# Performance work log

Measured on AMD Instinct MI355X. Metric: run time of the kernel, lower is better.

The kernel has to match this reference:

```python
import jax, jax.numpy as jnp
import numpy as np

USER_NUM = 100000
ITEM_NUM = 100000
N_NODES = USER_NUM + ITEM_NUM
EMB = 64
NNZ = 4000000
N_LAYERS = 3


def setup_inputs() -> dict:
    key = jax.random.key(0)
    k1, k2, k3, k4, k5 = jax.random.split(key, 5)
    # xavier-ish init for embeddings
    scale = np.sqrt(6.0 / (USER_NUM + EMB)).astype(np.float32)
    user_emb = jax.random.uniform(k1, (USER_NUM, EMB), jnp.float32, -scale, scale)
    item_emb = jax.random.uniform(k2, (ITEM_NUM, EMB), jnp.float32, -scale, scale)
    # COO sparse normalized adjacency: values ~ 1/deg scale
    adj_row = jax.random.randint(k3, (NNZ,), 0, N_NODES, dtype=jnp.int64)
    adj_col = jax.random.randint(k4, (NNZ,), 0, N_NODES, dtype=jnp.int64)
    adj_val = jax.random.uniform(k5, (NNZ,), jnp.float32) * (1.0 / 20.0)
    return {"user_emb": user_emb, "item_emb": item_emb,
            "adj_row": adj_row, "adj_col": adj_col, "adj_val": adj_val}


def _spmm(adj_row, adj_col, adj_val, x):
    # y[r] = sum_{e: row[e]==r} val[e] * x[col[e]]   (COO SpMM)
    msg = adj_val[:, None] * x[adj_col]  # [nnz, EMB]
    return jax.ops.segment_sum(msg, adj_row, num_segments=N_NODES)


def reference(user_emb, item_emb, adj_row, adj_col, adj_val):
    ego = jnp.concatenate([user_emb, item_emb], axis=0)  # [N, EMB]
    acc = jnp.zeros_like(ego)
    for _ in range(N_LAYERS):
        ego = _spmm(adj_row, adj_col, adj_val, ego)
        acc = acc + ego
    final = acc / N_LAYERS  # mean over stacked layer outputs
    return final[:USER_NUM], final[USER_NUM:]
```

## Files before the change

kernel.cpp:

```cpp
#include <hip/hip_runtime.h>
#include <hip/hip_fp16.h>

#define EMB 64
#define BROWS 128
#define BSHIFT 7
#define LDSN 2048
#define CHUNK 16384
#define SORT_CAP 5120

typedef int   iv4 __attribute__((ext_vector_type(4)));
typedef float fv4 __attribute__((ext_vector_type(4)));
typedef unsigned uv2 __attribute__((ext_vector_type(2)));

__global__ __launch_bounds__(1024) void bucket_hist(const int* __restrict__ rows,
                                                    int* __restrict__ counts,
                                                    int nnz, int nbuck) {
    __shared__ int lc[LDSN];
    for (int i = threadIdx.x; i < LDSN; i += 1024) lc[i] = 0;
    __syncthreads();
    int stride = gridDim.x * blockDim.x;
    int tid = blockIdx.x * blockDim.x + threadIdx.x;
    int n4 = nnz >> 2;
    for (int q = tid; q < n4; q += stride) {
        iv4 r = __builtin_nontemporal_load((const iv4*)rows + q);
        atomicAdd(&lc[r.x >> BSHIFT], 1);
        atomicAdd(&lc[r.y >> BSHIFT], 1);
        atomicAdd(&lc[r.z >> BSHIFT], 1);
        atomicAdd(&lc[r.w >> BSHIFT], 1);
    }
    int base = n4 << 2;
    if (tid < (nnz - base)) atomicAdd(&lc[rows[base + tid] >> BSHIFT], 1);
    __syncthreads();
    for (int i = threadIdx.x; i < nbuck; i += 1024) {
        int v = lc[i];
        if (v) atomicAdd(&counts[i], v);
    }
}

__global__ void scan_buckets(const int* __restrict__ counts, int* __restrict__ bstart,
                             int* __restrict__ cursor, int nbuck) {
    __shared__ int lds[256];
    int tid = threadIdx.x;
    int run = 0;
    for (int base = 0; base < nbuck; base += 256) {
        int idx = base + tid;
        int v = (idx < nbuck) ? counts[idx] : 0;
        int x = v;
        lds[tid] = x; __syncthreads();
        for (int off = 1; off < 256; off <<= 1) {
            int t = (tid >= off) ? lds[tid - off] : 0;
            __syncthreads();
            x += t; lds[tid] = x; __syncthreads();
        }
        if (idx < nbuck) { int ex = run + x - v; bstart[idx] = ex; cursor[idx] = ex; }
        int tot = lds[255];
        __syncthreads();
        run += tot;
    }
    if (tid == 0) bstart[nbuck] = run;
}

__global__ __launch_bounds__(1024) void bucket_scatter(
        const int* __restrict__ rows, const int* __restrict__ cols,
        const float* __restrict__ vals, int* __restrict__ cursor,
        int2* __restrict__ packed, int nnz) {
    __shared__ int lc[LDSN];
    __shared__ int lbase[LDSN];
    int base = blockIdx.x * CHUNK;
    int end = min(base + CHUNK, nnz);
    for (int i = threadIdx.x; i < LDSN; i += 1024) lc[i] = 0;
    __syncthreads();
    for (int i = base + threadIdx.x; i < end; i += 1024)
        atomicAdd(&lc[rows[i] >> BSHIFT], 1);
    __syncthreads();
    for (int i = threadIdx.x; i < LDSN; i += 1024) {
        int v = lc[i];
        lbase[i] = v ? atomicAdd(&cursor[i], v) : 0;
        lc[i] = 0;
    }
    __syncthreads();
    for (int i = base + threadIdx.x; i < end; i += 1024) {
        int r = rows[i];
        int bk = r >> BSHIFT;
        int slot = lbase[bk] + atomicAdd(&lc[bk], 1);
        packed[slot] = make_int2(cols[i] | ((r & (BROWS - 1)) << 18),
                                 __float_as_int(vals[i]));
    }
}

__global__ __launch_bounds__(512) void sort_bucket(
        int2* __restrict__ packed, const int* __restrict__ bstart,
        int* __restrict__ offs, int n_rows, int nbuck) {
    __shared__ int2 ebuf[SORT_CAP];
    __shared__ int cnt[BROWS];
    __shared__ int coff[BROWS];
    int b = blockIdx.x;
    int s = bstart[b], e = bstart[b + 1];
    int sz = e - s;
    int tid = threadIdx.x;
    if (tid < BROWS) cnt[tid] = 0;
    __syncthreads();
    for (int i = tid; i < sz; i += 512) {
        int2 ed = packed[s + i];
        ebuf[i] = ed;
        atomicAdd(&cnt[(ed.x >> 18) & (BROWS - 1)], 1);
    }
    __syncthreads();
    int v = (tid < BROWS) ? cnt[tid] : 0;
    if (tid < BROWS) coff[tid] = v;
    __syncthreads();
    for (int off = 1; off < BROWS; off <<= 1) {
        int add = (tid < BROWS && tid >= off) ? coff[tid - off] : 0;
        __syncthreads();
        if (tid < BROWS) coff[tid] += add;
        __syncthreads();
    }
    if (tid < BROWS) {
        int ex = coff[tid] - v;
        cnt[tid] = ex;
        int row = (b << BSHIFT) + tid;
        if (row < n_rows) offs[row] = s + ex;
    }
    if (b == nbuck - 1 && tid == 0) offs[n_rows] = e;
    __syncthreads();
    for (int i = tid; i < sz; i += 512) {
        int2 ed = ebuf[i];
        int rl = (ed.x >> 18) & (BROWS - 1);
        int pos = atomicAdd(&cnt[rl], 1);
        packed[s + pos] = make_int2(ed.x & 0x3FFFF, ed.y);
    }
}

__global__ __launch_bounds__(256) void cast_concat_half(
        const float* __restrict__ a, const float* __restrict__ b,
        int na4, int ntot4, __half* __restrict__ o) {
    int stride = gridDim.x * blockDim.x;
    for (int i = blockIdx.x * blockDim.x + threadIdx.x; i < ntot4; i += stride) {
        fv4 v = (i < na4) ? ((const fv4*)a)[i] : ((const fv4*)b)[i - na4];
        __half2 h0 = __floats2half2_rn(v.x, v.y);
        __half2 h1 = __floats2half2_rn(v.z, v.w);
        uv2 w;
        w.x = *(unsigned*)&h0;
        w.y = *(unsigned*)&h1;
        *((uv2*)o + i) = w;
    }
}

__global__ __launch_bounds__(256) void spmm_row_h(
        const int* __restrict__ offs, const int2* __restrict__ packed,
        const __half* __restrict__ xh,
        __half* __restrict__ yh, float* __restrict__ out, int n_rows, int mode) {
    int wid = (blockIdx.x * blockDim.x + threadIdx.x) >> 6;
    if (wid >= n_rows) return;
    int lane = threadIdx.x & 63;
    int r = __builtin_amdgcn_readfirstlane(wid);
    int s = offs[r];
    int e = offs[r + 1];
    const unsigned long long* pk = (const unsigned long long*)packed;
    float a0 = 0.f, a1 = 0.f, a2 = 0.f, a3 = 0.f;
    float a4 = 0.f, a5 = 0.f, a6 = 0.f, a7 = 0.f;
    int k = s;
    for (; k + 7 < e; k += 8) {
        unsigned long long w0 = __builtin_nontemporal_load(pk + k);
        unsigned long long w1 = __builtin_nontemporal_load(pk + k + 1);
        unsigned long long w2 = __builtin_nontemporal_load(pk + k + 2);
        unsigned long long w3 = __builtin_nontemporal_load(pk + k + 3);
        unsigned long long w4 = __builtin_nontemporal_load(pk + k + 4);
        unsigned long long w5 = __builtin_nontemporal_load(pk + k + 5);
        unsigned long long w6 = __builtin_nontemporal_load(pk + k + 6);
        unsigned long long w7 = __builtin_nontemporal_load(pk + k + 7);
        float h0 = __half2float(xh[(((int)(unsigned)w0) << 6) + lane]);
        float h1 = __half2float(xh[(((int)(unsigned)w1) << 6) + lane]);
        float h2 = __half2float(xh[(((int)(unsigned)w2) << 6) + lane]);
        float h3 = __half2float(xh[(((int)(unsigned)w3) << 6) + lane]);
        float h4 = __half2float(xh[(((int)(unsigned)w4) << 6) + lane]);
        float h5 = __half2float(xh[(((int)(unsigned)w5) << 6) + lane]);
        float h6 = __half2float(xh[(((int)(unsigned)w6) << 6) + lane]);
        float h7 = __half2float(xh[(((int)(unsigned)w7) << 6) + lane]);
        a0 += __int_as_float((int)(w0 >> 32)) * h0;
        a1 += __int_as_float((int)(w1 >> 32)) * h1;
        a2 += __int_as_float((int)(w2 >> 32)) * h2;
        a3 += __int_as_float((int)(w3 >> 32)) * h3;
        a4 += __int_as_float((int)(w4 >> 32)) * h4;
        a5 += __int_as_float((int)(w5 >> 32)) * h5;
        a6 += __int_as_float((int)(w6 >> 32)) * h6;
        a7 += __int_as_float((int)(w7 >> 32)) * h7;
    }
    for (; k + 3 < e; k += 4) {
        unsigned long long w0 = __builtin_nontemporal_load(pk + k);
        unsigned long long w1 = __builtin_nontemporal_load(pk + k + 1);
        unsigned long long w2 = __builtin_nontemporal_load(pk + k + 2);
        unsigned long long w3 = __builtin_nontemporal_load(pk + k + 3);
        float h0 = __half2float(xh[(((int)(unsigned)w0) << 6) + lane]);
        float h1 = __half2float(xh[(((int)(unsigned)w1) << 6) + lane]);
        float h2 = __half2float(xh[(((int)(unsigned)w2) << 6) + lane]);
        float h3 = __half2float(xh[(((int)(unsigned)w3) << 6) + lane]);
        a0 += __int_as_float((int)(w0 >> 32)) * h0;
        a1 += __int_as_float((int)(w1 >> 32)) * h1;
        a2 += __int_as_float((int)(w2 >> 32)) * h2;
        a3 += __int_as_float((int)(w3 >> 32)) * h3;
    }
    for (; k < e; ++k) {
        unsigned long long w = __builtin_nontemporal_load(pk + k);
        a0 += __int_as_float((int)(w >> 32)) *
              __half2float(xh[(((int)(unsigned)w) << 6) + lane]);
    }
    float acc = ((a0 + a1) + (a2 + a3)) + ((a4 + a5) + (a6 + a7));
    size_t oi = ((size_t)r << 6) + lane;
    if (mode == 0) {
        __builtin_nontemporal_store(acc, &out[oi]);
        yh[oi] = __float2half_rn(acc);
    } else if (mode == 1) {
        float o = __builtin_nontemporal_load(&out[oi]);
        __builtin_nontemporal_store(o + acc, &out[oi]);
        yh[oi] = __float2half_rn(acc);
    } else {
        float o = __builtin_nontemporal_load(&out[oi]);
        __builtin_nontemporal_store((o + acc) * (1.0f / 3.0f), &out[oi]);
    }
}

extern "C" void kernel_launch(void* const* d_in, const int* in_sizes, int n_in,
                              void* d_out, int out_size, void* d_ws, size_t ws_size,
                              hipStream_t stream) {
    const float* user_emb = (const float*)d_in[0];
    const float* item_emb = (const float*)d_in[1];
    const int*   adj_row  = (const int*)d_in[2];
    const int*   adj_col  = (const int*)d_in[3];
    const float* adj_val  = (const float*)d_in[4];
    float* out = (float*)d_out;

    const int n_user = in_sizes[0] / EMB;
    const int n_item = in_sizes[1] / EMB;
    const int n      = n_user + n_item;
    const int nnz    = in_sizes[2];
    const size_t half_bytes = (size_t)n * EMB * sizeof(__half);
    const int nbuck  = (n + BROWS - 1) >> BSHIFT;

    char* p = (char*)d_ws;
    __half* X0    = (__half*)p; p += half_bytes;
    __half* Ah    = (__half*)p; p += half_bytes;
    __half* Bh    = (__half*)p; p += half_bytes;
    int2*  packed = (int2*)p;  p += (size_t)nnz * sizeof(int2);
    int*   offs   = (int*)p;   p += (size_t)(n + 1) * sizeof(int);
    int*   bstart = (int*)p;   p += (size_t)(nbuck + 1) * sizeof(int);
    int*   cursor = (int*)p;   p += (size_t)nbuck * sizeof(int);
    int*   counts = (int*)p;   p += (size_t)nbuck * sizeof(int);

    cast_concat_half<<<2048, 256, 0, stream>>>(user_emb, item_emb,
                                               n_user * EMB / 4, n * EMB / 4, X0);

    hipMemsetAsync(counts, 0, (size_t)nbuck * sizeof(int), stream);
    bucket_hist<<<256, 1024, 0, stream>>>(adj_row, counts, nnz, nbuck);
    scan_buckets<<<1, 256, 0, stream>>>(counts, bstart, cursor, nbuck);
    bucket_scatter<<<(nnz + CHUNK - 1) / CHUNK, 1024, 0, stream>>>(
        adj_row, adj_col, adj_val, cursor, packed, nnz);
    sort_bucket<<<nbuck, 512, 0, stream>>>(packed, bstart, offs, n, nbuck);

    const int sgrid = (n * EMB + 255) / 256;
    spmm_row_h<<<sgrid, 256, 0, stream>>>(offs, packed, X0, Ah, out, n, 0);
    spmm_row_h<<<sgrid, 256, 0, stream>>>(offs, packed, Ah, Bh, out, n, 1);
    spmm_row_h<<<sgrid, 256, 0, stream>>>(offs, packed, Bh, Bh, out, n, 2);
}
```

Measured before the change: 577.6 us.

## Reuse per-chunk histograms in scatter and vectorize COO loads

The histogram kernel now runs per CHUNK and writes each chunk's bucket counts to a workspace table. The scatter kernel reads that table instead of re-reading the row array and rebuilding the local histogram, and it loads rows, cols and vals as 4-wide nontemporal vectors. sort_bucket moves from 512 to 1024 threads per block. The cost is an extra nchunk*2048 int workspace table and its write and read traffic.

Result: faster. 548.6 us (-5.0%).

```diff
diff --git a/kernel.cpp b/kernel.cpp
--- a/kernel.cpp
+++ b/kernel.cpp
@@ -12,27 +12,30 @@
 typedef float fv4 __attribute__((ext_vector_type(4)));
 typedef unsigned uv2 __attribute__((ext_vector_type(2)));
 
-__global__ __launch_bounds__(1024) void bucket_hist(const int* __restrict__ rows,
-                                                    int* __restrict__ counts,
-                                                    int nnz, int nbuck) {
+__global__ __launch_bounds__(1024) void hist_chunk(const int* __restrict__ rows,
+                                                   int* __restrict__ counts,
+                                                   int* __restrict__ ccnt,
+                                                   int nnz, int nbuck) {
     __shared__ int lc[LDSN];
     for (int i = threadIdx.x; i < LDSN; i += 1024) lc[i] = 0;
     __syncthreads();
-    int stride = gridDim.x * blockDim.x;
-    int tid = blockIdx.x * blockDim.x + threadIdx.x;
-    int n4 = nnz >> 2;
-    for (int q = tid; q < n4; q += stride) {
-        iv4 r = __builtin_nontemporal_load((const iv4*)rows + q);
+    int base = blockIdx.x * CHUNK;
+    int end  = min(base + CHUNK, nnz);
+    int nfull = (end - base) & ~3;
+    for (int i = base + threadIdx.x * 4; i < base + nfull; i += 4096) {
+        iv4 r = __builtin_nontemporal_load((const iv4*)rows + (i >> 2));
         atomicAdd(&lc[r.x >> BSHIFT], 1);
         atomicAdd(&lc[r.y >> BSHIFT], 1);
         atomicAdd(&lc[r.z >> BSHIFT], 1);
         atomicAdd(&lc[r.w >> BSHIFT], 1);
     }
-    int base = n4 << 2;
-    if (tid < (nnz - base)) atomicAdd(&lc[rows[base + tid] >> BSHIFT], 1);
-    __syncthreads();
+    int t = base + nfull + threadIdx.x;
+    if (t < end) atomicAdd(&lc[rows[t] >> BSHIFT], 1);
+    __syncthreads();
+    size_t crow = (size_t)blockIdx.x * LDSN;
     for (int i = threadIdx.x; i < nbuck; i += 1024) {
         int v = lc[i];
+        ccnt[crow + i] = v;
         if (v) atomicAdd(&counts[i], v);
     }
 }
@@ -62,33 +65,47 @@
 
 __global__ __launch_bounds__(1024) void bucket_scatter(
         const int* __restrict__ rows, const int* __restrict__ cols,
-        const float* __restrict__ vals, int* __restrict__ cursor,
-        int2* __restrict__ packed, int nnz) {
+        const float* __restrict__ vals, const int* __restrict__ ccnt,
+        int* __restrict__ cursor, int2* __restrict__ packed, int nnz, int nbuck) {
     __shared__ int lc[LDSN];
     __shared__ int lbase[LDSN];
-    int base = blockIdx.x * CHUNK;
-    int end = min(base + CHUNK, nnz);
-    for (int i = threadIdx.x; i < LDSN; i += 1024) lc[i] = 0;
-    __syncthreads();
-    for (int i = base + threadIdx.x; i < end; i += 1024)
-        atomicAdd(&lc[rows[i] >> BSHIFT], 1);
-    __syncthreads();
-    for (int i = threadIdx.x; i < LDSN; i += 1024) {
-        int v = lc[i];
+    int chunk = blockIdx.x;
+    int base = chunk * CHUNK;
+    int end  = min(base + CHUNK, nnz);
+    size_t crow = (size_t)chunk * LDSN;
+    for (int i = threadIdx.x; i < nbuck; i += 1024) {
+        int v = ccnt[crow + i];
         lbase[i] = v ? atomicAdd(&cursor[i], v) : 0;
         lc[i] = 0;
     }
     __syncthreads();
-    for (int i = base + threadIdx.x; i < end; i += 1024) {
-        int r = rows[i];
+    int nfull = (end - base) & ~3;
+    for (int i = base + threadIdx.x * 4; i < base + nfull; i += 4096) {
+        iv4 r = __builtin_nontemporal_load((const iv4*)rows + (i >> 2));
+        iv4 c = __builtin_nontemporal_load((const iv4*)cols + (i >> 2));
+        fv4 v = __builtin_nontemporal_load((const fv4*)vals + (i >> 2));
+        int bk0 = r.x >> BSHIFT, bk1 = r.y >> BSHIFT;
+        int bk2 = r.z >> BSHIFT, bk3 = r.w >> BSHIFT;
+        int s0 = lbase[bk0] + atomicAdd(&lc[bk0], 1);
+        int s1 = lbase[bk1] + atomicAdd(&lc[bk1], 1);
+        int s2 = lbase[bk2] + atomicAdd(&lc[bk2], 1);
+        int s3 = lbase[bk3] + atomicAdd(&lc[bk3], 1);
+        packed[s0] = make_int2(c.x | ((r.x & (BROWS - 1)) << 18), __float_as_int(v.x));
+        packed[s1] = make_int2(c.y | ((r.y & (BROWS - 1)) << 18), __float_as_int(v.y));
+        packed[s2] = make_int2(c.z | ((r.z & (BROWS - 1)) << 18), __float_as_int(v.z));
+        packed[s3] = make_int2(c.w | ((r.w & (BROWS - 1)) << 18), __float_as_int(v.w));
+    }
+    int t = base + nfull + threadIdx.x;
+    if (t < end) {
+        int r = rows[t];
         int bk = r >> BSHIFT;
         int slot = lbase[bk] + atomicAdd(&lc[bk], 1);
-        packed[slot] = make_int2(cols[i] | ((r & (BROWS - 1)) << 18),
-                                 __float_as_int(vals[i]));
-    }
-}
-
-__global__ __launch_bounds__(512) void sort_bucket(
+        packed[slot] = make_int2(cols[t] | ((r & (BROWS - 1)) << 18),
+                                 __float_as_int(vals[t]));
+    }
+}
+
+__global__ __launch_bounds__(1024) void sort_bucket(
         int2* __restrict__ packed, const int* __restrict__ bstart,
         int* __restrict__ offs, int n_rows, int nbuck) {
     __shared__ int2 ebuf[SORT_CAP];
@@ -100,7 +117,7 @@
     int tid = threadIdx.x;
     if (tid < BROWS) cnt[tid] = 0;
     __syncthreads();
-    for (int i = tid; i < sz; i += 512) {
+    for (int i = tid; i < sz; i += 1024) {
         int2 ed = packed[s + i];
         ebuf[i] = ed;
         atomicAdd(&cnt[(ed.x >> 18) & (BROWS - 1)], 1);
@@ -123,7 +140,7 @@
     }
     if (b == nbuck - 1 && tid == 0) offs[n_rows] = e;
     __syncthreads();
-    for (int i = tid; i < sz; i += 512) {
+    for (int i = tid; i < sz; i += 1024) {
         int2 ed = ebuf[i];
         int rl = (ed.x >> 18) & (BROWS - 1);
         int pos = atomicAdd(&cnt[rl], 1);
@@ -236,6 +253,7 @@
     const int nnz    = in_sizes[2];
     const size_t half_bytes = (size_t)n * EMB * sizeof(__half);
     const int nbuck  = (n + BROWS - 1) >> BSHIFT;
+    const int nchunk = (nnz + CHUNK - 1) / CHUNK;
 
     char* p = (char*)d_ws;
     __half* X0    = (__half*)p; p += half_bytes;
@@ -246,16 +264,17 @@
     int*   bstart = (int*)p;   p += (size_t)(nbuck + 1) * sizeof(int);
     int*   cursor = (int*)p;   p += (size_t)nbuck * sizeof(int);
     int*   counts = (int*)p;   p += (size_t)nbuck * sizeof(int);
+    int*   ccnt   = (int*)p;   p += (size_t)nchunk * LDSN * sizeof(int);
 
     cast_concat_half<<<2048, 256, 0, stream>>>(user_emb, item_emb,
                                                n_user * EMB / 4, n * EMB / 4, X0);
 
     hipMemsetAsync(counts, 0, (size_t)nbuck * sizeof(int), stream);
-    bucket_hist<<<256, 1024, 0, stream>>>(adj_row, counts, nnz, nbuck);
+    hist_chunk<<<nchunk, 1024, 0, stream>>>(adj_row, counts, ccnt, nnz, nbuck);
     scan_buckets<<<1, 256, 0, stream>>>(counts, bstart, cursor, nbuck);
-    bucket_scatter<<<(nnz + CHUNK - 1) / CHUNK, 1024, 0, stream>>>(
-        adj_row, adj_col, adj_val, cursor, packed, nnz);
-    sort_bucket<<<nbuck, 512, 0, stream>>>(packed, bstart, offs, n, nbuck);
+    bucket_scatter<<<nchunk, 1024, 0, stream>>>(adj_row, adj_col, adj_val,
+                                                ccnt, cursor, packed, nnz, nbuck);
+    sort_bucket<<<nbuck, 1024, 0, stream>>>(packed, bstart, offs, n, nbuck);
 
     const int sgrid = (n * EMB + 255) / 256;
     spmm_row_h<<<sgrid, 256, 0, stream>>>(offs, packed, X0, Ah, out, n, 0);
```
